# Kernel optimization log

Hardware: AMD Instinct MI355X
Metric: run time of the kernel (lower is better)

The kernel has to match this reference:

```python
import jax, jax.numpy as jnp
import numpy as np

N_IN = 100000
N_OUT = 100000
E = 1600000
C_IN = 1
C_MID = 64
C_OUT = 64
POS_DIM = 3


def setup_inputs() -> dict:
    key = jax.random.key(0)
    ks = jax.random.split(key, 10)
    x_in = jax.random.normal(ks[0], (N_IN, C_IN), dtype=jnp.float32)
    pos_in = jax.random.uniform(ks[1], (N_IN, POS_DIM), dtype=jnp.float32)
    batch_in = jnp.zeros((N_IN,), dtype=jnp.int64)
    pos_out = jax.random.uniform(ks[2], (N_OUT, POS_DIM), dtype=jnp.float32)
    in_index = jax.random.randint(ks[3], (E,), 0, N_IN, dtype=jnp.int64)
    out_index = jnp.sort(jax.random.randint(ks[4], (E,), 0, N_OUT, dtype=jnp.int64))
    # parameters (Linear weights stored as [in, out] for x @ W)
    s1 = 1.0 / np.sqrt(POS_DIM)
    s2 = 1.0 / np.sqrt(16)
    s3 = 1.0 / np.sqrt(C_MID * C_IN)
    W1 = jax.random.uniform(ks[5], (POS_DIM, 16), dtype=jnp.float32, minval=-s1, maxval=s1)
    W2 = jax.random.uniform(ks[6], (16, C_MID), dtype=jnp.float32, minval=-s2, maxval=s2)
    W3 = jax.random.uniform(ks[7], (C_MID * C_IN, C_OUT), dtype=jnp.float32, minval=-s3, maxval=s3)
    b3 = jax.random.uniform(ks[8], (C_OUT,), dtype=jnp.float32, minval=-s3, maxval=s3)
    return {"x_in": x_in, "pos_in": pos_in, "batch_in": batch_in, "pos_out": pos_out,
            "in_index": in_index, "out_index": out_index,
            "W1": W1, "W2": W2, "W3": W3, "b3": b3}


def reference(x_in, pos_in, batch_in, pos_out, in_index, out_index, W1, W2, W3, b3):
    n_out = pos_out.shape[0]
    # gather relative positions per edge: [E, pos_dim]
    pos_local = pos_in[in_index] - pos_out[out_index]
    # per-edge MLP on geometry
    M = jax.nn.celu(pos_local @ W1)          # [E, 16]
    M = jax.nn.celu(M @ W2)                  # [E, c_mid]
    # gather node features per edge
    x_edge = x_in[in_index]                  # [E, c_in]
    # degree normalization (clamped to >= 1)
    deg = jax.ops.segment_sum(jnp.ones((out_index.shape[0],), dtype=pos_in.dtype),
                              out_index, num_segments=n_out)
    deg = jnp.maximum(deg, 1.0)
    x_edge = x_edge / deg[out_index][:, None]
    # outer product and scatter-sum into output nodes
    outer = jnp.einsum('ei,ej->eij', x_edge, M)  # [E, c_in, c_mid]
    agg = jax.ops.segment_sum(outer.reshape(outer.shape[0], -1), out_index,
                              num_segments=n_out)  # [N_out, c_in*c_mid]
    out = agg @ W3 + b3
    out = jnp.nan_to_num(out, nan=0.0, posinf=1e6, neginf=-1e6)
    return out
```

## Files before the change

### kernel.cpp

```cpp
#include <hip/hip_runtime.h>
#include <math.h>


typedef __attribute__((ext_vector_type(8))) short short8;
typedef __attribute__((ext_vector_type(4))) float f32x4;
typedef __attribute__((ext_vector_type(4))) int   int4v;
typedef __attribute__((ext_vector_type(2))) int   int2v;

union frag_u { int i[4]; short8 v; };

__device__ __forceinline__ float celu1(float x) {
    float m = fminf(x, 0.0f);
    return fmaxf(x, __expf(m) - 1.0f);
}
__device__ __forceinline__ int cvt_pk_bf16(float lo, float hi) {
    int r; asm("v_cvt_pk_bf16_f32 %0, %1, %2" : "=v"(r) : "v"(lo), "v"(hi)); return r;
}

__global__ void k_zero_start(const int* __restrict__ oi, int* __restrict__ start,
                             f32x4* __restrict__ agg4, int n_out, int E, int nzero4,
                             const float* __restrict__ pos_in,
                             const float* __restrict__ x_in,
                             f32x4* __restrict__ pos4, int n_in) {
    const int t = blockIdx.x * blockDim.x + threadIdx.x;
    if (t <= E) {
        const int cur  = (t < E) ? oi[t] : n_out;
        const int prev = (t > 0) ? oi[t - 1] : -1;
        for (int o = prev + 1; o <= cur; ++o) start[o] = t;
    }
    if (pos4 != nullptr && t < n_in) {
        f32x4 v;
        v.x = pos_in[t*3+0]; v.y = pos_in[t*3+1]; v.z = pos_in[t*3+2];
        v.w = x_in[t];
        pos4[t] = v;
    }
    const f32x4 z = {0.f, 0.f, 0.f, 0.f};
    for (int i = t; i < nzero4; i += gridDim.x * blockDim.x) agg4[i] = z;
}

template<bool P4>
__global__ __launch_bounds__(256) void k_edges(
    const float* __restrict__ x_in, const float* __restrict__ pos_in,
    const f32x4* __restrict__ pos4,
    const float* __restrict__ pos_out, const int* __restrict__ in_index,
    const int* __restrict__ out_index,
    const float* __restrict__ W1, const float* __restrict__ W2,
    float* __restrict__ agg, int E, int nwin, int totwaves)
{
    __shared__ int   hbuf [4][64][10];
    __shared__ float scoef[4][64];
    __shared__ int   srank[4][64];
    __shared__ int   snid [4][64];

    const int wv = threadIdx.x >> 6, lane = threadIdx.x & 63;
    const int kcol = lane & 15, q = lane >> 4;

    frag_u b1[4];
#pragma unroll
    for (int jt = 0; jt < 4; ++jt) {
        const int j = jt * 16 + kcol;
        b1[jt].i[0] = cvt_pk_bf16(W2[(4*q+0)*64 + j], W2[(4*q+1)*64 + j]);
        b1[jt].i[1] = cvt_pk_bf16(W2[(4*q+2)*64 + j], W2[(4*q+3)*64 + j]);
        b1[jt].i[2] = 0; b1[jt].i[3] = 0;
    }
    const f32x4 zero4 = {0.f, 0.f, 0.f, 0.f};

    for (int win = blockIdx.x * 4 + wv; win < nwin; win += totwaves) {
        const int e = win * 64 + lane;
        const bool valid = e < E;
        const int ec = valid ? e : E - 1;

        const int node = out_index[ec];
        const int idx  = in_index[ec];

        float xv, pix, piy, piz;
        if (P4) {
            const f32x4 pv = pos4[idx];
            pix = pv.x; piy = pv.y; piz = pv.z; xv = pv.w;
        } else {
            xv  = x_in[idx];
            pix = pos_in[idx*3+0]; piy = pos_in[idx*3+1]; piz = pos_in[idx*3+2];
        }
        const float coef = valid ? xv : 0.0f;
        const float px = pix - pos_out[node*3+0];
        const float py = piy - pos_out[node*3+1];
        const float pz = piz - pos_out[node*3+2];

        int hp[8];
#pragma unroll
        for (int c = 0; c < 8; ++c) {
            const float h0 = celu1(fmaf(pz, W1[32 + 2*c],     fmaf(py, W1[16 + 2*c],     px * W1[2*c])));
            const float h1 = celu1(fmaf(pz, W1[32 + 2*c + 1], fmaf(py, W1[16 + 2*c + 1], px * W1[2*c + 1])));
            hp[c] = cvt_pk_bf16(h0, h1);
        }
        *(int4v*)&hbuf[wv][lane][0] = *(const int4v*)&hp[0];
        *(int4v*)&hbuf[wv][lane][4] = *(const int4v*)&hp[4];

        const int prevn = __shfl_up(node, 1);
        const bool head = (kcol == 0) || (node != prevn);
        const unsigned long long bal = __ballot(head);
        const unsigned mym = (unsigned)(bal >> (q * 16)) & 0xFFFFu;
        const int rank = __popc(mym & ((2u << kcol) - 1)) - 1;

        scoef[wv][lane] = coef;
        srank[wv][lane] = rank;
        if (head) snid[wv][(lane & 48) + rank] = node;

        int ndq[4];
#pragma unroll
        for (int Q = 0; Q < 4; ++Q) ndq[Q] = __popc((unsigned)(bal >> (Q * 16)) & 0xFFFFu);

#pragma unroll
        for (int Q = 0; Q < 4; ++Q) {
            const int2v a1lo = *(const int2v*)&hbuf[wv][Q*16 + kcol][2*q];
            frag_u a1; a1.i[0] = a1lo.x; a1.i[1] = a1lo.y; a1.i[2] = 0; a1.i[3] = 0;

            const f32x4 c4 = *(const f32x4*)&scoef[wv][Q*16 + 4*q];
            const int4v r4 = *(const int4v*)&srank[wv][Q*16 + 4*q];
            const int4v n4 = *(const int4v*)&snid [wv][Q*16 + 4*q];

            frag_u a2;
            a2.i[0] = cvt_pk_bf16(r4.x == kcol ? c4.x : 0.0f, r4.y == kcol ? c4.y : 0.0f);
            a2.i[1] = cvt_pk_bf16(r4.z == kcol ? c4.z : 0.0f, r4.w == kcol ? c4.w : 0.0f);
            a2.i[2] = 0; a2.i[3] = 0;

            const int nd = ndq[Q];
            float* p0 = agg + (long)n4.x * 64 + kcol;
            float* p1 = agg + (long)n4.y * 64 + kcol;
            float* p2 = agg + (long)n4.z * 64 + kcol;
            float* p3 = agg + (long)n4.w * 64 + kcol;

#pragma unroll
            for (int jt = 0; jt < 4; ++jt) {
                f32x4 d1 = __builtin_amdgcn_mfma_f32_16x16x32_bf16(a1.v, b1[jt].v, zero4, 0, 0, 0);
                frag_u b2;
                b2.i[0] = cvt_pk_bf16(celu1(d1[0]), celu1(d1[1]));
                b2.i[1] = cvt_pk_bf16(celu1(d1[2]), celu1(d1[3]));
                b2.i[2] = 0; b2.i[3] = 0;
                f32x4 d2 = __builtin_amdgcn_mfma_f32_16x16x32_bf16(a2.v, b2.v, zero4, 0, 0, 0);
                if (4*q + 0 < nd) unsafeAtomicAdd(p0 + jt * 16, d2[0]);
                if (4*q + 1 < nd) unsafeAtomicAdd(p1 + jt * 16, d2[1]);
                if (4*q + 2 < nd) unsafeAtomicAdd(p2 + jt * 16, d2[2]);
                if (4*q + 3 < nd) unsafeAtomicAdd(p3 + jt * 16, d2[3]);
            }
        }
    }
}

__global__ __launch_bounds__(256) void k_out(
    float* __restrict__ agg, const float* __restrict__ W3,
    const float* __restrict__ b3, const int* __restrict__ start,
    int n_out, int ntiles, int totwaves)
{
    const int wv = threadIdx.x >> 6, lane = threadIdx.x & 63;
    const int s = lane & 15, q = lane >> 4;

    frag_u B0[4], B1[4];
    float bias[4];
#pragma unroll
    for (int jt = 0; jt < 4; ++jt) {
        const int j = jt * 16 + s;
        bias[jt] = b3[j];
        B0[jt].i[0] = cvt_pk_bf16(W3[( 4*q+0)*64+j], W3[( 4*q+1)*64+j]);
        B0[jt].i[1] = cvt_pk_bf16(W3[( 4*q+2)*64+j], W3[( 4*q+3)*64+j]);
        B0[jt].i[2] = cvt_pk_bf16(W3[(16+4*q+0)*64+j], W3[(16+4*q+1)*64+j]);
        B0[jt].i[3] = cvt_pk_bf16(W3[(16+4*q+2)*64+j], W3[(16+4*q+3)*64+j]);
        B1[jt].i[0] = cvt_pk_bf16(W3[(32+4*q+0)*64+j], W3[(32+4*q+1)*64+j]);
        B1[jt].i[1] = cvt_pk_bf16(W3[(32+4*q+2)*64+j], W3[(32+4*q+3)*64+j]);
        B1[jt].i[2] = cvt_pk_bf16(W3[(48+4*q+0)*64+j], W3[(48+4*q+1)*64+j]);
        B1[jt].i[3] = cvt_pk_bf16(W3[(48+4*q+2)*64+j], W3[(48+4*q+3)*64+j]);
    }
    const f32x4 zero4 = {0.f, 0.f, 0.f, 0.f};

    for (int tile = blockIdx.x * 4 + wv; tile < ntiles; tile += totwaves) {
        const long base = (long)tile * 16;

        const long row_i = base + s;
        const long row_c = row_i < n_out ? row_i : n_out - 1;
        const float* row = agg + row_c * 64;
        const int dd = start[row_c + 1] - start[row_c];
        const float invd = 1.0f / (float)(dd > 0 ? dd : 1);

        f32x4 r0 = *(const f32x4*)(row +      4*q);
        f32x4 r1 = *(const f32x4*)(row + 16 + 4*q);
        f32x4 r2 = *(const f32x4*)(row + 32 + 4*q);
        f32x4 r3 = *(const f32x4*)(row + 48 + 4*q);
        r0 *= invd; r1 *= invd; r2 *= invd; r3 *= invd;

        frag_u A0, A1;
        A0.i[0] = cvt_pk_bf16(r0.x, r0.y); A0.i[1] = cvt_pk_bf16(r0.z, r0.w);
        A0.i[2] = cvt_pk_bf16(r1.x, r1.y); A0.i[3] = cvt_pk_bf16(r1.z, r1.w);
        A1.i[0] = cvt_pk_bf16(r2.x, r2.y); A1.i[1] = cvt_pk_bf16(r2.z, r2.w);
        A1.i[2] = cvt_pk_bf16(r3.x, r3.y); A1.i[3] = cvt_pk_bf16(r3.z, r3.w);

#pragma unroll
        for (int jt = 0; jt < 4; ++jt) {
            f32x4 d = __builtin_amdgcn_mfma_f32_16x16x32_bf16(A0.v, B0[jt].v, zero4, 0, 0, 0);
            d = __builtin_amdgcn_mfma_f32_16x16x32_bf16(A1.v, B1[jt].v, d, 0, 0, 0);
            const int j = jt * 16 + s;
#pragma unroll
            for (int r = 0; r < 4; ++r) {
                const long nodei = base + 4*q + r;
                if (nodei < n_out) {
                    float v = d[r] + bias[jt];
                    if (isnan(v)) v = 0.0f;
                    else if (isinf(v)) v = (v > 0.0f) ? 1e6f : -1e6f;
                    agg[nodei * 64 + j] = v;
                }
            }
        }
    }
}

extern "C" void kernel_launch(void* const* d_in, const int* in_sizes, int n_in_args,
                              void* d_out, int out_size, void* d_ws, size_t ws_size,
                              hipStream_t stream) {
    const float* x_in      = (const float*)d_in[0];
    const float* pos_in    = (const float*)d_in[1];
    const float* pos_out   = (const float*)d_in[3];
    const int*   in_index  = (const int*)d_in[4];
    const int*   out_index = (const int*)d_in[5];
    const float* W1        = (const float*)d_in[6];
    const float* W2        = (const float*)d_in[7];
    const float* W3        = (const float*)d_in[8];
    const float* b3        = (const float*)d_in[9];
    float* out = (float*)d_out;

    const int n_out = in_sizes[3] / 3;
    const int E     = in_sizes[4];
    const int n_in  = in_sizes[0];

    int* start = (int*)d_ws;
    const size_t start_bytes = ((size_t)(n_out + 1) * 4 + 255) & ~(size_t)255;
    const size_t need = start_bytes + (size_t)n_in * 16;
    const bool use_p4 = (ws_size >= need);
    f32x4* pos4 = use_p4 ? (f32x4*)((char*)d_ws + start_bytes) : nullptr;

    {
        const int nzero4 = n_out * 16;
        int span = (E + 1) > nzero4 ? (E + 1) : nzero4;
        if (n_in > span) span = n_in;
        dim3 b(256), g((span + 255) / 256);
        k_zero_start<<<g, b, 0, stream>>>(out_index, start, (f32x4*)out, n_out, E,
                                          nzero4, pos_in, x_in, pos4, n_in);
    }

    {
        const int nwin = (E + 63) / 64;
        const int nblocks = (nwin + 7) / 8;
        const int totwaves = nblocks * 4;
        if (use_p4)
            k_edges<true><<<dim3(nblocks), dim3(256), 0, stream>>>(
                x_in, pos_in, pos4, pos_out, in_index, out_index, W1, W2, out, E, nwin, totwaves);
        else
            k_edges<false><<<dim3(nblocks), dim3(256), 0, stream>>>(
                x_in, pos_in, pos4, pos_out, in_index, out_index, W1, W2, out, E, nwin, totwaves);
    }
    {
        const int ntiles = (n_out + 15) / 16;
        const int nblocks = (ntiles + 7) / 8;
        const int totwaves = nblocks * 4;
        k_out<<<dim3(nblocks), dim3(256), 0, stream>>>(
            out, W3, b3, start, n_out, ntiles, totwaves);
    }
}
```

Baseline: 77.30 us.

## Merge per-quarter segment partials in LDS before writing global aggregate

Per-window segment results are accumulated into a shared-memory tile indexed by wave-level segment rank, using LDS atomics across the four 16-lane quarters. Each segment row is then written once to global memory: a plain store for segments fully inside the window, and an atomic only for the first and last segments. This targets the large volume of global float atomics from repeated quarter-level heads. In exchange it adds LDS zeroing, LDS atomics and about 35KB of shared memory per block, which may lower occupancy; windows with more than 32 segments fall back to the old path.

```diff
diff --git a/kernel.cpp b/kernel.cpp
--- a/kernel.cpp
+++ b/kernel.cpp
@@ -51,6 +51,8 @@
     __shared__ float scoef[4][64];
     __shared__ int   srank[4][64];
     __shared__ int   snid [4][64];
+    __shared__ int   snidw[4][32];
+    __shared__ float acc  [4][32][68];
 
     const int wv = threadIdx.x >> 6, lane = threadIdx.x & 63;
     const int kcol = lane & 15, q = lane >> 4;
@@ -97,51 +99,100 @@
         *(int4v*)&hbuf[wv][lane][4] = *(const int4v*)&hp[4];
 
         const int prevn = __shfl_up(node, 1);
-        const bool head = (kcol == 0) || (node != prevn);
-        const unsigned long long bal = __ballot(head);
-        const unsigned mym = (unsigned)(bal >> (q * 16)) & 0xFFFFu;
+        const bool whead = (lane == 0) || (node != prevn);
+        const unsigned long long wbal = __ballot(whead);
+        const int ndw = __popcll(wbal);
+        const unsigned long long qbal = wbal | 0x0001000100010001ULL;
+        const unsigned mym = (unsigned)(qbal >> (q * 16)) & 0xFFFFu;
         const int rank = __popc(mym & ((2u << kcol) - 1)) - 1;
 
         scoef[wv][lane] = coef;
         srank[wv][lane] = rank;
-        if (head) snid[wv][(lane & 48) + rank] = node;
+        const bool qhead = (qbal >> lane) & 1ull;
+        if (qhead) snid[wv][(lane & 48) + rank] = node;
+        const int wrank = __popcll(wbal & ((2ULL << lane) - 1)) - 1;
+        if (whead && wrank < 32) snidw[wv][wrank] = node;
 
         int ndq[4];
 #pragma unroll
-        for (int Q = 0; Q < 4; ++Q) ndq[Q] = __popc((unsigned)(bal >> (Q * 16)) & 0xFFFFu);
-
-#pragma unroll
-        for (int Q = 0; Q < 4; ++Q) {
-            const int2v a1lo = *(const int2v*)&hbuf[wv][Q*16 + kcol][2*q];
-            frag_u a1; a1.i[0] = a1lo.x; a1.i[1] = a1lo.y; a1.i[2] = 0; a1.i[3] = 0;
-
-            const f32x4 c4 = *(const f32x4*)&scoef[wv][Q*16 + 4*q];
-            const int4v r4 = *(const int4v*)&srank[wv][Q*16 + 4*q];
-            const int4v n4 = *(const int4v*)&snid [wv][Q*16 + 4*q];
-
-            frag_u a2;
-            a2.i[0] = cvt_pk_bf16(r4.x == kcol ? c4.x : 0.0f, r4.y == kcol ? c4.y : 0.0f);
-            a2.i[1] = cvt_pk_bf16(r4.z == kcol ? c4.z : 0.0f, r4.w == kcol ? c4.w : 0.0f);
-            a2.i[2] = 0; a2.i[3] = 0;
-
-            const int nd = ndq[Q];
-            float* p0 = agg + (long)n4.x * 64 + kcol;
-            float* p1 = agg + (long)n4.y * 64 + kcol;
-            float* p2 = agg + (long)n4.z * 64 + kcol;
-            float* p3 = agg + (long)n4.w * 64 + kcol;
-
-#pragma unroll
-            for (int jt = 0; jt < 4; ++jt) {
-                f32x4 d1 = __builtin_amdgcn_mfma_f32_16x16x32_bf16(a1.v, b1[jt].v, zero4, 0, 0, 0);
-                frag_u b2;
-                b2.i[0] = cvt_pk_bf16(celu1(d1[0]), celu1(d1[1]));
-                b2.i[1] = cvt_pk_bf16(celu1(d1[2]), celu1(d1[3]));
-                b2.i[2] = 0; b2.i[3] = 0;
-                f32x4 d2 = __builtin_amdgcn_mfma_f32_16x16x32_bf16(a2.v, b2.v, zero4, 0, 0, 0);
-                if (4*q + 0 < nd) unsafeAtomicAdd(p0 + jt * 16, d2[0]);
-                if (4*q + 1 < nd) unsafeAtomicAdd(p1 + jt * 16, d2[1]);
-                if (4*q + 2 < nd) unsafeAtomicAdd(p2 + jt * 16, d2[2]);
-                if (4*q + 3 < nd) unsafeAtomicAdd(p3 + jt * 16, d2[3]);
+        for (int Q = 0; Q < 4; ++Q) ndq[Q] = __popc((unsigned)(qbal >> (Q * 16)) & 0xFFFFu);
+
+        if (ndw <= 32) {
+            for (int s = 0; s < ndw; ++s) acc[wv][s][lane] = 0.0f;
+
+#pragma unroll
+            for (int Q = 0; Q < 4; ++Q) {
+                const int2v a1lo = *(const int2v*)&hbuf[wv][Q*16 + kcol][2*q];
+                frag_u a1; a1.i[0] = a1lo.x; a1.i[1] = a1lo.y; a1.i[2] = 0; a1.i[3] = 0;
+
+                const f32x4 c4 = *(const f32x4*)&scoef[wv][Q*16 + 4*q];
+                const int4v r4 = *(const int4v*)&srank[wv][Q*16 + 4*q];
+
+                frag_u a2;
+                a2.i[0] = cvt_pk_bf16(r4.x == kcol ? c4.x : 0.0f, r4.y == kcol ? c4.y : 0.0f);
+                a2.i[1] = cvt_pk_bf16(r4.z == kcol ? c4.z : 0.0f, r4.w == kcol ? c4.w : 0.0f);
+                a2.i[2] = 0; a2.i[3] = 0;
+
+                const int nd = ndq[Q];
+                const int rowQ = __popcll(wbal & ((1ULL << (Q*16 + 1)) - 1)) - 1;
+
+#pragma unroll
+                for (int jt = 0; jt < 4; ++jt) {
+                    f32x4 d1 = __builtin_amdgcn_mfma_f32_16x16x32_bf16(a1.v, b1[jt].v, zero4, 0, 0, 0);
+                    frag_u b2;
+                    b2.i[0] = cvt_pk_bf16(celu1(d1[0]), celu1(d1[1]));
+                    b2.i[1] = cvt_pk_bf16(celu1(d1[2]), celu1(d1[3]));
+                    b2.i[2] = 0; b2.i[3] = 0;
+                    f32x4 d2 = __builtin_amdgcn_mfma_f32_16x16x32_bf16(a2.v, b2.v, zero4, 0, 0, 0);
+                    const int colj = jt * 16 + kcol;
+                    if (4*q + 0 < nd) atomicAdd(&acc[wv][rowQ + 4*q + 0][colj], d2[0]);
+                    if (4*q + 1 < nd) atomicAdd(&acc[wv][rowQ + 4*q + 1][colj], d2[1]);
+                    if (4*q + 2 < nd) atomicAdd(&acc[wv][rowQ + 4*q + 2][colj], d2[2]);
+                    if (4*q + 3 < nd) atomicAdd(&acc[wv][rowQ + 4*q + 3][colj], d2[3]);
+                }
+            }
+
+            for (int s = 0; s < ndw; ++s) {
+                const int ns = snidw[wv][s];
+                const float v = acc[wv][s][lane];
+                float* p = agg + (long)ns * 64 + lane;
+                if (s == 0 || s == ndw - 1) unsafeAtomicAdd(p, v);
+                else *p = v;
+            }
+        } else {
+#pragma unroll
+            for (int Q = 0; Q < 4; ++Q) {
+                const int2v a1lo = *(const int2v*)&hbuf[wv][Q*16 + kcol][2*q];
+                frag_u a1; a1.i[0] = a1lo.x; a1.i[1] = a1lo.y; a1.i[2] = 0; a1.i[3] = 0;
+
+                const f32x4 c4 = *(const f32x4*)&scoef[wv][Q*16 + 4*q];
+                const int4v r4 = *(const int4v*)&srank[wv][Q*16 + 4*q];
+                const int4v n4 = *(const int4v*)&snid [wv][Q*16 + 4*q];
+
+                frag_u a2;
+                a2.i[0] = cvt_pk_bf16(r4.x == kcol ? c4.x : 0.0f, r4.y == kcol ? c4.y : 0.0f);
+                a2.i[1] = cvt_pk_bf16(r4.z == kcol ? c4.z : 0.0f, r4.w == kcol ? c4.w : 0.0f);
+                a2.i[2] = 0; a2.i[3] = 0;
+
+                const int nd = ndq[Q];
+                float* p0 = agg + (long)n4.x * 64 + kcol;
+                float* p1 = agg + (long)n4.y * 64 + kcol;
+                float* p2 = agg + (long)n4.z * 64 + kcol;
+                float* p3 = agg + (long)n4.w * 64 + kcol;
+
+#pragma unroll
+                for (int jt = 0; jt < 4; ++jt) {
+                    f32x4 d1 = __builtin_amdgcn_mfma_f32_16x16x32_bf16(a1.v, b1[jt].v, zero4, 0, 0, 0);
+                    frag_u b2;
+                    b2.i[0] = cvt_pk_bf16(celu1(d1[0]), celu1(d1[1]));
+                    b2.i[1] = cvt_pk_bf16(celu1(d1[2]), celu1(d1[3]));
+                    b2.i[2] = 0; b2.i[3] = 0;
+                    f32x4 d2 = __builtin_amdgcn_mfma_f32_16x16x32_bf16(a2.v, b2.v, zero4, 0, 0, 0);
+                    if (4*q + 0 < nd) unsafeAtomicAdd(p0 + jt * 16, d2[0]);
+                    if (4*q + 1 < nd) unsafeAtomicAdd(p1 + jt * 16, d2[1]);
+                    if (4*q + 2 < nd) unsafeAtomicAdd(p2 + jt * 16, d2[2]);
+                    if (4*q + 3 < nd) unsafeAtomicAdd(p3 + jt * 16, d2[3]);
+                }
             }
         }
     }
```

Measured after the change: 112.7 us. 1.46x slower.
